# Optimization experiments

Measured on AMD Instinct MI355X. Metric: run time of the kernel, lower is better.

Reference implementation:

```python
import jax, jax.numpy as jnp
import numpy as np

KERNEL_SIZE = 11
SIGMA = 1.5
DATA_RANGE = 1.0
C1 = (0.01 * DATA_RANGE) ** 2
C2 = (0.03 * DATA_RANGE) ** 2


def _gaussian_kernel_2d(kernel_size=KERNEL_SIZE, sigma=SIGMA):
    coords = jnp.arange(kernel_size, dtype=jnp.float32) - kernel_size // 2
    g1d = jnp.exp(-coords ** 2 / (2.0 * sigma ** 2))
    g2d = g1d[:, None] * g1d[None, :]
    return g2d / g2d.sum()  # [K, K]


def _depthwise_blur(x, kernel2d):
    # x: [B, C, H, W]; kernel2d: [K, K] -> depthwise conv, SAME padding
    C = x.shape[1]
    k = jnp.broadcast_to(kernel2d[None, None], (C, 1, KERNEL_SIZE, KERNEL_SIZE)).astype(x.dtype)
    pad = KERNEL_SIZE // 2
    return jax.lax.conv_general_dilated(
        x, k,
        window_strides=(1, 1),
        padding=((pad, pad), (pad, pad)),
        dimension_numbers=('NCHW', 'OIHW', 'NCHW'),
        feature_group_count=C,
    )


def reference(pred, target):
    kernel2d = _gaussian_kernel_2d()
    mu_p = _depthwise_blur(pred, kernel2d)
    mu_t = _depthwise_blur(target, kernel2d)
    mu_p_sq = mu_p * mu_p
    mu_t_sq = mu_t * mu_t
    mu_pt = mu_p * mu_t
    sigma_p_sq = _depthwise_blur(pred * pred, kernel2d) - mu_p_sq
    sigma_t_sq = _depthwise_blur(target * target, kernel2d) - mu_t_sq
    sigma_pt = _depthwise_blur(pred * target, kernel2d) - mu_pt
    sigma_p_sq = jnp.clip(sigma_p_sq, 0.0, None)
    sigma_t_sq = jnp.clip(sigma_t_sq, 0.0, None)
    numerator = (2.0 * mu_pt + C1) * (2.0 * sigma_pt + C2)
    denominator = (mu_p_sq + mu_t_sq + C1) * (sigma_p_sq + sigma_t_sq + C2)
    ssim_map = numerator / denominator
    return 1.0 - jnp.mean(ssim_map)


def setup_inputs() -> dict:
    key = jax.random.key(0)
    k1, k2 = jax.random.split(key)
    shape = (16, 3, 512, 512)
    pred = jax.random.uniform(k1, shape, dtype=jnp.float32)
    target = jax.random.uniform(k2, shape, dtype=jnp.float32)
    return {"pred": pred, "target": target}
```

## Files before the change

### kernel.cpp

```cpp
#include <hip/hip_runtime.h>
#include <hip/hip_fp16.h>


#define WIDTH  512
#define HEIGHT 512
#define TW 64
#define SH 128
#define RING 48
#define RST 56
#define TILES_X 8
#define TILES_Y (HEIGHT / SH)
#define PLANES 48
#define NBLK (TILES_X * TILES_Y * PLANES)
#define NPIXF 12582912.0f

typedef _Float16 half8_t __attribute__((ext_vector_type(8)));
typedef float f32x4_t __attribute__((ext_vector_type(4)));
typedef unsigned int u32x4_t __attribute__((ext_vector_type(4)));

__device__ __forceinline__ float wsel(int i) {
    unsigned a = (unsigned)i;
    float r = 0.f;
    if (a == 5u)              r = 0.26601168f;
    if (a == 4u || a == 6u)   r = 0.21300566f;
    if (a == 3u || a == 7u)   r = 0.10936069f;
    if (a == 2u || a == 8u)   r = 0.03600077f;
    if (a == 1u || a == 9u)   r = 0.00759881f;
    if (a == 0u || a == 10u)  r = 0.00102839f;
    return r;
}

__global__ __launch_bounds__(256)
void ssim_main(const float* __restrict__ pred,
               const float* __restrict__ tgt,
               float* __restrict__ partial) {
    __shared__ __align__(16) __half s_ring[4][TW][RST];
    __shared__ __align__(16) __half s_pl[4][16][88];
    __shared__ __align__(16) float  s_raw[2][2][16][80];
    __shared__ float s_red[4];

    const int tid  = threadIdx.x;
    const int wv   = tid >> 6;
    const int lane = tid & 63;
    const int r15  = lane & 15;
    const int g4   = lane >> 4;
    const int x0 = blockIdx.x * TW;
    const int y0 = blockIdx.y * SH;
    const size_t plane_off = (size_t)blockIdx.z * (WIDTH * HEIGHT);
    const float* P = pred + plane_off;
    const float* T = tgt + plane_off;
    const bool x_int = (x0 >= 8) && (x0 + TW + 8 <= WIDTH);

    const float s1 = 2.f * ((float)(_Float16)0.00102839f + (float)(_Float16)0.00759881f
                   + (float)(_Float16)0.03600077f + (float)(_Float16)0.10936069f
                   + (float)(_Float16)0.21300566f) + (float)(_Float16)0.26601168f;
    const float cs = 1.f / (s1 * s1);

    half8_t Bh, Bv;
#pragma unroll
    for (int jj = 0; jj < 8; ++jj) {
        int k = g4 * 8 + jj;
        Bv[jj] = (_Float16)wsel(k - r15);
        Bh[jj] = (_Float16)wsel(k - r15 - 3);
    }

    auto issue_async = [&](int buf, int gybase) {
#pragma unroll 1
        for (int l = wv; l < 10; l += 4) {
            int fi  = l * 256 + lane * 4;
            int arr = fi / 1280;
            int rem = fi - arr * 1280;
            int row = rem / 80;
            int col = rem - row * 80;
            int gy = gybase + row;
            if (gy < 0) gy = 0;
            if (gy > HEIGHT - 1) gy = HEIGHT - 1;
            int gx = x0 - 8 + col;
            if (gx < 0) gx = 0;
            if (gx > WIDTH - 4) gx = WIDTH - 4;
            const float* src = (arr == 0 ? P : T) + ((size_t)gy << 9) + gx;
            char* ldsbase = (char*)&s_raw[buf][0][0][0] + l * 1024;
            __builtin_amdgcn_global_load_lds(
                (const __attribute__((address_space(1))) unsigned int*)(const void*)src,
                (__attribute__((address_space(3))) unsigned int*)(void*)ldsbase,
                16, 0, 0);
        }
    };

    auto elementwise = [&](int buf, int gybase) {
        auto do_quad = [&](int row, int cq) {
            int gy = gybase + row;
            float4 pv = *(const float4*)&s_raw[buf][0][row][cq * 4];
            float4 tv = *(const float4*)&s_raw[buf][1][row][cq * 4];
            if ((unsigned)gy >= (unsigned)HEIGHT) {
                pv.x = pv.y = pv.z = pv.w = 0.f;
                tv.x = tv.y = tv.z = tv.w = 0.f;
            } else if (!x_int) {
                int gx0 = x0 - 8 + cq * 4;
                if ((unsigned)(gx0 + 0) >= (unsigned)WIDTH) { pv.x = 0.f; tv.x = 0.f; }
                if ((unsigned)(gx0 + 1) >= (unsigned)WIDTH) { pv.y = 0.f; tv.y = 0.f; }
                if ((unsigned)(gx0 + 2) >= (unsigned)WIDTH) { pv.z = 0.f; tv.z = 0.f; }
                if ((unsigned)(gx0 + 3) >= (unsigned)WIDTH) { pv.w = 0.f; tv.w = 0.f; }
            }
            float u0 = fmaf(pv.x, pv.x, tv.x * tv.x), v0 = pv.x * tv.x;
            float u1 = fmaf(pv.y, pv.y, tv.y * tv.y), v1 = pv.y * tv.y;
            float u2 = fmaf(pv.z, pv.z, tv.z * tv.z), v2 = pv.z * tv.z;
            float u3 = fmaf(pv.w, pv.w, tv.w * tv.w), v3 = pv.w * tv.w;
            uint2 wp, wt, wu, wvv;
            wp.x  = __builtin_bit_cast(unsigned, __floats2half2_rn(pv.x, pv.y));
            wp.y  = __builtin_bit_cast(unsigned, __floats2half2_rn(pv.z, pv.w));
            wt.x  = __builtin_bit_cast(unsigned, __floats2half2_rn(tv.x, tv.y));
            wt.y  = __builtin_bit_cast(unsigned, __floats2half2_rn(tv.z, tv.w));
            wu.x  = __builtin_bit_cast(unsigned, __floats2half2_rn(u0, u1));
            wu.y  = __builtin_bit_cast(unsigned, __floats2half2_rn(u2, u3));
            wvv.x = __builtin_bit_cast(unsigned, __floats2half2_rn(v0, v1));
            wvv.y = __builtin_bit_cast(unsigned, __floats2half2_rn(v2, v3));
            *(uint2*)&s_pl[0][row][cq * 4] = wp;
            *(uint2*)&s_pl[1][row][cq * 4] = wt;
            *(uint2*)&s_pl[2][row][cq * 4] = wu;
            *(uint2*)&s_pl[3][row][cq * 4] = wvv;
        };
        do_quad(tid >> 4, tid & 15);
        if (tid < 64) do_quad(tid >> 2, 16 + (tid & 3));
    };

    auto hblur_store = [&](int relbase) {
        int s0 = relbase + 4 * g4;
        if (s0 >= 96) s0 -= 96;
        if (s0 >= 48) s0 -= 48;
        int s1b = s0 + 2; if (s1b >= 48) s1b -= 48;
        const int colA = (wv << 4) + r15;
        const int acol = (wv << 4) + g4 * 8;
#pragma unroll
        for (int q = 0; q < 4; ++q) {
            u32x4_t ra = *(const u32x4_t*)&s_pl[q][r15][acol];
            f32x4_t z = {0.f, 0.f, 0.f, 0.f};
            f32x4_t d = __builtin_amdgcn_mfma_f32_16x16x32_f16(
                __builtin_bit_cast(half8_t, ra), Bh, z, 0, 0, 0);
            unsigned p01 = __builtin_bit_cast(unsigned, __floats2half2_rn(d[0], d[1]));
            unsigned p23 = __builtin_bit_cast(unsigned, __floats2half2_rn(d[2], d[3]));
            *(unsigned*)&s_ring[q][colA][s0]  = p01;
            *(unsigned*)&s_ring[q][colA][s1b] = p23;
        }
    };

    float lsum = 0.f;

    auto vblur_ssim = [&](int jstep) {
        int sg = 16 * jstep + 8 * g4;
        if (sg >= 96) sg -= 96;
        if (sg >= 48) sg -= 48;
        const int colA = (wv << 4) + r15;
        f32x4_t acc[4];
#pragma unroll
        for (int q = 0; q < 4; ++q) {
            u32x4_t ra = *(const u32x4_t*)&s_ring[q][colA][sg];
            f32x4_t z = {0.f, 0.f, 0.f, 0.f};
            acc[q] = __builtin_amdgcn_mfma_f32_16x16x32_f16(
                __builtin_bit_cast(half8_t, ra), Bv, z, 0, 0, 0);
        }
#pragma unroll
        for (int r = 0; r < 4; ++r) {
            float mp = acc[0][r] * cs, mt = acc[1][r] * cs;
            float U  = acc[2][r] * cs, V  = acc[3][r] * cs;
            float mpt = mp * mt;
            float B2  = fmaf(mp, mp, mt * mt);
            float spt  = V - mpt;
            float ssum = U - B2;
            float num = fmaf(2.f, mpt, 1e-4f) * fmaf(2.f, spt, 9e-4f);
            float den = (B2 + 1e-4f) * (ssum + 9e-4f);
            lsum += __fdividef(num, den);
        }
    };

    issue_async(0, y0 - 5);
    {
        u32x4_t z4 = {0u, 0u, 0u, 0u};
#pragma unroll 1
        for (int i = tid; i < (int)(sizeof(s_ring) / 16); i += 256)
            ((u32x4_t*)s_ring)[i] = z4;
    }
    __syncthreads();
    issue_async(1, y0 + 5);
    elementwise(0, y0 - 5);
    __syncthreads();
    hblur_store(0);
    __syncthreads();
    issue_async(0, y0 + 21);
    elementwise(1, y0 + 5);
    __syncthreads();
    hblur_store(10);
    __syncthreads();

#pragma unroll 1
    for (int j = 0; j < 8; ++j) {
        if (j < 6) issue_async((j + 1) & 1, y0 + 16 * (j + 1) + 21);
        if (j < 7) elementwise(j & 1, y0 + 16 * j + 21);
        vblur_ssim(j);
        __syncthreads();
        if (j < 7) hblur_store(16 * j + 26);
        __syncthreads();
    }

#pragma unroll
    for (int off = 32; off > 0; off >>= 1) lsum += __shfl_down(lsum, off);
    if ((tid & 63) == 0) s_red[tid >> 6] = lsum;
    __syncthreads();
    if (tid == 0) {
        partial[(blockIdx.z * TILES_Y + blockIdx.y) * TILES_X + blockIdx.x] =
            s_red[0] + s_red[1] + s_red[2] + s_red[3];
    }
}

__global__ __launch_bounds__(256)
void ssim_final(const float* __restrict__ partial, float* __restrict__ out) {
    __shared__ float s_red[4];
    float s = 0.f;
    for (int i = threadIdx.x; i < NBLK; i += 256) s += partial[i];
#pragma unroll
    for (int off = 32; off > 0; off >>= 1) s += __shfl_down(s, off);
    if ((threadIdx.x & 63) == 0) s_red[threadIdx.x >> 6] = s;
    __syncthreads();
    if (threadIdx.x == 0) {
        float total = s_red[0] + s_red[1] + s_red[2] + s_red[3];
        out[0] = 1.0f - total / NPIXF;
    }
}

extern "C" void kernel_launch(void* const* d_in, const int* in_sizes, int n_in,
                              void* d_out, int out_size, void* d_ws, size_t ws_size,
                              hipStream_t stream) {
    const float* pred = (const float*)d_in[0];
    const float* tgt  = (const float*)d_in[1];
    float* partial = (float*)d_ws;

    dim3 grid(TILES_X, TILES_Y, PLANES);
    ssim_main<<<grid, dim3(256), 0, stream>>>(pred, tgt, partial);
    ssim_final<<<1, dim3(256), 0, stream>>>(partial, (float*)d_out);
}
```

Before: 153.2 us.

## Replace async LDS staging with register-prefetched loads and restructure blur pipeline

Removes the global_load_lds double-buffered raw staging and instead prefetches the next 16-row strip directly into registers, overlapping the loads with hblur/vblur MFMA work. LDS use shrinks, and launch bounds now request 4 waves per SIMD to raise occupancy. The row offsets shift (7/23/28 instead of 5/21/26) to pair with a single 8-byte ring store. The SSIM constants are also folded so the per-pixel normalisation multiplies drop out. This adds register pressure, and the changed ring offsets and scaling put correctness at risk.

Result: faster. 130.6 us (-14.7%).

```diff
diff --git a/kernel.cpp b/kernel.cpp
--- a/kernel.cpp
+++ b/kernel.cpp
@@ -30,13 +30,12 @@
     return r;
 }
 
-__global__ __launch_bounds__(256)
+__global__ __launch_bounds__(256, 4)
 void ssim_main(const float* __restrict__ pred,
                const float* __restrict__ tgt,
                float* __restrict__ partial) {
     __shared__ __align__(16) __half s_ring[4][TW][RST];
-    __shared__ __align__(16) __half s_pl[4][16][88];
-    __shared__ __align__(16) float  s_raw[2][2][16][80];
+    __shared__ __align__(16) __half s_pl[4][16][80];
     __shared__ float s_red[4];
 
     const int tid  = threadIdx.x;
@@ -54,7 +53,9 @@
     const float s1 = 2.f * ((float)(_Float16)0.00102839f + (float)(_Float16)0.00759881f
                    + (float)(_Float16)0.03600077f + (float)(_Float16)0.10936069f
                    + (float)(_Float16)0.21300566f) + (float)(_Float16)0.26601168f;
-    const float cs = 1.f / (s1 * s1);
+    const float a   = s1 * s1;
+    const float C1A = a * a * 1e-4f;
+    const float C2A = a * a * 9e-4f;
 
     half8_t Bh, Bv;
 #pragma unroll
@@ -64,92 +65,85 @@
         Bh[jj] = (_Float16)wsel(k - r15 - 3);
     }
 
-    auto issue_async = [&](int buf, int gybase) {
-#pragma unroll 1
-        for (int l = wv; l < 10; l += 4) {
-            int fi  = l * 256 + lane * 4;
-            int arr = fi / 1280;
-            int rem = fi - arr * 1280;
-            int row = rem / 80;
-            int col = rem - row * 80;
-            int gy = gybase + row;
-            if (gy < 0) gy = 0;
-            if (gy > HEIGHT - 1) gy = HEIGHT - 1;
-            int gx = x0 - 8 + col;
-            if (gx < 0) gx = 0;
-            if (gx > WIDTH - 4) gx = WIDTH - 4;
-            const float* src = (arr == 0 ? P : T) + ((size_t)gy << 9) + gx;
-            char* ldsbase = (char*)&s_raw[buf][0][0][0] + l * 1024;
-            __builtin_amdgcn_global_load_lds(
-                (const __attribute__((address_space(1))) unsigned int*)(const void*)src,
-                (__attribute__((address_space(3))) unsigned int*)(void*)ldsbase,
-                16, 0, 0);
-        }
-    };
-
-    auto elementwise = [&](int buf, int gybase) {
-        auto do_quad = [&](int row, int cq) {
-            int gy = gybase + row;
-            float4 pv = *(const float4*)&s_raw[buf][0][row][cq * 4];
-            float4 tv = *(const float4*)&s_raw[buf][1][row][cq * 4];
-            if ((unsigned)gy >= (unsigned)HEIGHT) {
-                pv.x = pv.y = pv.z = pv.w = 0.f;
-                tv.x = tv.y = tv.z = tv.w = 0.f;
-            } else if (!x_int) {
-                int gx0 = x0 - 8 + cq * 4;
-                if ((unsigned)(gx0 + 0) >= (unsigned)WIDTH) { pv.x = 0.f; tv.x = 0.f; }
-                if ((unsigned)(gx0 + 1) >= (unsigned)WIDTH) { pv.y = 0.f; tv.y = 0.f; }
-                if ((unsigned)(gx0 + 2) >= (unsigned)WIDTH) { pv.z = 0.f; tv.z = 0.f; }
-                if ((unsigned)(gx0 + 3) >= (unsigned)WIDTH) { pv.w = 0.f; tv.w = 0.f; }
-            }
-            float u0 = fmaf(pv.x, pv.x, tv.x * tv.x), v0 = pv.x * tv.x;
-            float u1 = fmaf(pv.y, pv.y, tv.y * tv.y), v1 = pv.y * tv.y;
-            float u2 = fmaf(pv.z, pv.z, tv.z * tv.z), v2 = pv.z * tv.z;
-            float u3 = fmaf(pv.w, pv.w, tv.w * tv.w), v3 = pv.w * tv.w;
-            uint2 wp, wt, wu, wvv;
-            wp.x  = __builtin_bit_cast(unsigned, __floats2half2_rn(pv.x, pv.y));
-            wp.y  = __builtin_bit_cast(unsigned, __floats2half2_rn(pv.z, pv.w));
-            wt.x  = __builtin_bit_cast(unsigned, __floats2half2_rn(tv.x, tv.y));
-            wt.y  = __builtin_bit_cast(unsigned, __floats2half2_rn(tv.z, tv.w));
-            wu.x  = __builtin_bit_cast(unsigned, __floats2half2_rn(u0, u1));
-            wu.y  = __builtin_bit_cast(unsigned, __floats2half2_rn(u2, u3));
-            wvv.x = __builtin_bit_cast(unsigned, __floats2half2_rn(v0, v1));
-            wvv.y = __builtin_bit_cast(unsigned, __floats2half2_rn(v2, v3));
-            *(uint2*)&s_pl[0][row][cq * 4] = wp;
-            *(uint2*)&s_pl[1][row][cq * 4] = wt;
-            *(uint2*)&s_pl[2][row][cq * 4] = wu;
-            *(uint2*)&s_pl[3][row][cq * 4] = wvv;
-        };
-        do_quad(tid >> 4, tid & 15);
-        if (tid < 64) do_quad(tid >> 2, 16 + (tid & 3));
-    };
-
-    auto hblur_store = [&](int relbase) {
+    const int  erow0 = tid >> 4, ecq0 = tid & 15;
+    const bool e2    = tid < 64;
+    const int  erow1 = tid >> 2, ecq1 = 16 + (tid & 3);
+
+    auto ldquad = [&](int gybase, int row, int cq, float4& p, float4& t) {
+        int gy = gybase + row;
+        if (gy < 0) gy = 0;
+        if (gy > HEIGHT - 1) gy = HEIGHT - 1;
+        int gx = x0 - 8 + cq * 4;
+        if (gx < 0) gx = 0;
+        if (gx > WIDTH - 4) gx = WIDTH - 4;
+        const size_t ro = (size_t)gy << 9;
+        p = *(const float4*)(P + ro + gx);
+        t = *(const float4*)(T + ro + gx);
+    };
+    auto load_gen = [&](int gybase, float4& p0, float4& t0,
+                        float4& p1, float4& t1) {
+        ldquad(gybase, erow0, ecq0, p0, t0);
+        if (e2) ldquad(gybase, erow1, ecq1, p1, t1);
+    };
+
+    auto equad = [&](int gybase, int row, int cq, float4 pv, float4 tv) {
+        int gy = gybase + row;
+        if ((unsigned)gy >= (unsigned)HEIGHT) {
+            pv.x = pv.y = pv.z = pv.w = 0.f;
+            tv.x = tv.y = tv.z = tv.w = 0.f;
+        } else if (!x_int) {
+            int gx0 = x0 - 8 + cq * 4;
+            if ((unsigned)(gx0 + 0) >= (unsigned)WIDTH) { pv.x = 0.f; tv.x = 0.f; }
+            if ((unsigned)(gx0 + 1) >= (unsigned)WIDTH) { pv.y = 0.f; tv.y = 0.f; }
+            if ((unsigned)(gx0 + 2) >= (unsigned)WIDTH) { pv.z = 0.f; tv.z = 0.f; }
+            if ((unsigned)(gx0 + 3) >= (unsigned)WIDTH) { pv.w = 0.f; tv.w = 0.f; }
+        }
+        float u0 = fmaf(pv.x, pv.x, tv.x * tv.x), v0 = pv.x * tv.x;
+        float u1 = fmaf(pv.y, pv.y, tv.y * tv.y), v1 = pv.y * tv.y;
+        float u2 = fmaf(pv.z, pv.z, tv.z * tv.z), v2 = pv.z * tv.z;
+        float u3 = fmaf(pv.w, pv.w, tv.w * tv.w), v3 = pv.w * tv.w;
+        uint2 wp, wt, wu, wvv;
+        wp.x  = __builtin_bit_cast(unsigned, __floats2half2_rn(pv.x, pv.y));
+        wp.y  = __builtin_bit_cast(unsigned, __floats2half2_rn(pv.z, pv.w));
+        wt.x  = __builtin_bit_cast(unsigned, __floats2half2_rn(tv.x, tv.y));
+        wt.y  = __builtin_bit_cast(unsigned, __floats2half2_rn(tv.z, tv.w));
+        wu.x  = __builtin_bit_cast(unsigned, __floats2half2_rn(u0, u1));
+        wu.y  = __builtin_bit_cast(unsigned, __floats2half2_rn(u2, u3));
+        wvv.x = __builtin_bit_cast(unsigned, __floats2half2_rn(v0, v1));
+        wvv.y = __builtin_bit_cast(unsigned, __floats2half2_rn(v2, v3));
+        *(uint2*)&s_pl[0][row][cq * 4] = wp;
+        *(uint2*)&s_pl[1][row][cq * 4] = wt;
+        *(uint2*)&s_pl[2][row][cq * 4] = wu;
+        *(uint2*)&s_pl[3][row][cq * 4] = wvv;
+    };
+    auto ewise = [&](int gybase, float4 p0, float4 t0, float4 p1, float4 t1) {
+        equad(gybase, erow0, ecq0, p0, t0);
+        if (e2) equad(gybase, erow1, ecq1, p1, t1);
+    };
+
+    auto hblur = [&](int relbase) {
         int s0 = relbase + 4 * g4;
-        if (s0 >= 96) s0 -= 96;
-        if (s0 >= 48) s0 -= 48;
-        int s1b = s0 + 2; if (s1b >= 48) s1b -= 48;
+        if (s0 >= 96) s0 -= 96; else if (s0 >= 48) s0 -= 48;
         const int colA = (wv << 4) + r15;
-        const int acol = (wv << 4) + g4 * 8;
+        const int acol = (wv << 4) + (g4 << 3);
 #pragma unroll
         for (int q = 0; q < 4; ++q) {
             u32x4_t ra = *(const u32x4_t*)&s_pl[q][r15][acol];
             f32x4_t z = {0.f, 0.f, 0.f, 0.f};
             f32x4_t d = __builtin_amdgcn_mfma_f32_16x16x32_f16(
                 __builtin_bit_cast(half8_t, ra), Bh, z, 0, 0, 0);
-            unsigned p01 = __builtin_bit_cast(unsigned, __floats2half2_rn(d[0], d[1]));
-            unsigned p23 = __builtin_bit_cast(unsigned, __floats2half2_rn(d[2], d[3]));
-            *(unsigned*)&s_ring[q][colA][s0]  = p01;
-            *(unsigned*)&s_ring[q][colA][s1b] = p23;
+            uint2 pk;
+            pk.x = __builtin_bit_cast(unsigned, __floats2half2_rn(d[0], d[1]));
+            pk.y = __builtin_bit_cast(unsigned, __floats2half2_rn(d[2], d[3]));
+            *(uint2*)&s_ring[q][colA][s0] = pk;
         }
     };
 
     float lsum = 0.f;
 
-    auto vblur_ssim = [&](int jstep) {
-        int sg = 16 * jstep + 8 * g4;
-        if (sg >= 96) sg -= 96;
-        if (sg >= 48) sg -= 48;
+    auto vblur = [&](int jstep) {
+        int sg = 16 * jstep + (g4 << 3);
+        if (sg >= 96) sg -= 96; else if (sg >= 48) sg -= 48;
         const int colA = (wv << 4) + r15;
         f32x4_t acc[4];
 #pragma unroll
@@ -161,44 +155,45 @@
         }
 #pragma unroll
         for (int r = 0; r < 4; ++r) {
-            float mp = acc[0][r] * cs, mt = acc[1][r] * cs;
-            float U  = acc[2][r] * cs, V  = acc[3][r] * cs;
-            float mpt = mp * mt;
-            float B2  = fmaf(mp, mp, mt * mt);
-            float spt  = V - mpt;
-            float ssum = U - B2;
-            float num = fmaf(2.f, mpt, 1e-4f) * fmaf(2.f, spt, 9e-4f);
-            float den = (B2 + 1e-4f) * (ssum + 9e-4f);
+            float mp = acc[0][r], mt = acc[1][r];
+            float U  = acc[2][r], V  = acc[3][r];
+            float mpt  = mp * mt;
+            float B2   = fmaf(mp, mp, mt * mt);
+            float S    = fmaf(a, V, -mpt);
+            float Ssum = fmaf(a, U, -B2);
+            float num = fmaf(2.f, mpt, C1A) * fmaf(2.f, S, C2A);
+            float den = (B2 + C1A) * (Ssum + C2A);
             lsum += __fdividef(num, den);
         }
     };
 
-    issue_async(0, y0 - 5);
+    float4 ap0, at0, ap1, at1;
+    float4 bp0, bt0, bp1, bt1;
+    load_gen(y0 - 5, ap0, at0, ap1, at1);
+    load_gen(y0 + 7, bp0, bt0, bp1, bt1);
     {
         u32x4_t z4 = {0u, 0u, 0u, 0u};
-#pragma unroll 1
-        for (int i = tid; i < (int)(sizeof(s_ring) / 16); i += 256)
-            ((u32x4_t*)s_ring)[i] = z4;
-    }
-    __syncthreads();
-    issue_async(1, y0 + 5);
-    elementwise(0, y0 - 5);
-    __syncthreads();
-    hblur_store(0);
-    __syncthreads();
-    issue_async(0, y0 + 21);
-    elementwise(1, y0 + 5);
-    __syncthreads();
-    hblur_store(10);
+#pragma unroll
+        for (int i = 0; i < 7; ++i)
+            ((u32x4_t*)s_ring)[tid + 256 * i] = z4;
+    }
+    ewise(y0 - 5, ap0, at0, ap1, at1);
+    __syncthreads();
+    hblur(0);
+    load_gen(y0 + 23, ap0, at0, ap1, at1);
+    __syncthreads();
+    ewise(y0 + 7, bp0, bt0, bp1, bt1);
+    __syncthreads();
+    hblur(12);
     __syncthreads();
 
 #pragma unroll 1
     for (int j = 0; j < 8; ++j) {
-        if (j < 6) issue_async((j + 1) & 1, y0 + 16 * (j + 1) + 21);
-        if (j < 7) elementwise(j & 1, y0 + 16 * j + 21);
-        vblur_ssim(j);
+        if (j < 7) ewise(y0 + 16 * j + 23, ap0, at0, ap1, at1);
         __syncthreads();
-        if (j < 7) hblur_store(16 * j + 26);
+        if (j < 6) load_gen(y0 + 16 * (j + 1) + 23, ap0, at0, ap1, at1);
+        if (j < 7) hblur(16 * j + 28);
+        vblur(j);
         __syncthreads();
     }
 
```
